# Optimization experiments

Hardware: AMD Instinct MI355X
Metric: run time of the kernel (lower is better)

The kernel has to match this reference:

```python
import jax, jax.numpy as jnp
import numpy as np

N, E = 50000, 800000
IN_DIM, HID, HEADS, OUT_DIM, EDGE_DIM = 128, 32, 4, 64, 32


def _glorot(key, shape, dtype=jnp.float32):
    fan_in, fan_out = shape[0], shape[1]
    lim = np.sqrt(6.0 / (fan_in + fan_out))
    return jax.random.uniform(key, shape, dtype, -lim, lim)


def setup_inputs() -> dict:
    key = jax.random.key(0)
    ks = jax.random.split(key, 16)
    H1 = HEADS * HID  # 128 = concat width of layer 1
    inp = {
        "x": jax.random.normal(ks[0], (N, IN_DIM), jnp.float32),
        "edge_index": jax.random.randint(ks[1], (2, E), 0, N, jnp.int64),
        "edge_feats": jax.random.normal(ks[2], (E, EDGE_DIM), jnp.float32),
        # layer 1: TransformerConv(128 -> 32, heads=4, concat=True, edge_dim=32)
        "Wq1": _glorot(ks[3], (IN_DIM, H1)), "bq1": jnp.zeros((H1,), jnp.float32),
        "Wk1": _glorot(ks[4], (IN_DIM, H1)), "bk1": jnp.zeros((H1,), jnp.float32),
        "Wv1": _glorot(ks[5], (IN_DIM, H1)), "bv1": jnp.zeros((H1,), jnp.float32),
        "We1": _glorot(ks[6], (EDGE_DIM, H1)),
        "Ws1": _glorot(ks[7], (IN_DIM, H1)), "bs1": jnp.zeros((H1,), jnp.float32),
        # layer 2: TransformerConv(128 -> 64, heads=1, concat=False, edge_dim=32)
        "Wq2": _glorot(ks[8], (H1, OUT_DIM)), "bq2": jnp.zeros((OUT_DIM,), jnp.float32),
        "Wk2": _glorot(ks[9], (H1, OUT_DIM)), "bk2": jnp.zeros((OUT_DIM,), jnp.float32),
        "Wv2": _glorot(ks[10], (H1, OUT_DIM)), "bv2": jnp.zeros((OUT_DIM,), jnp.float32),
        "We2": _glorot(ks[11], (EDGE_DIM, OUT_DIM)),
        "Ws2": _glorot(ks[12], (H1, OUT_DIM)), "bs2": jnp.zeros((OUT_DIM,), jnp.float32),
    }
    return inp


def _tconv(x, src, dst, e, Wq, bq, Wk, bk, Wv, bv, We, Ws, bs, heads, concat):
    """PyG TransformerConv: gather q_i/k_j/v_j, add edge embedding to k and v,
    segment-softmax over incoming edges of each target node, scatter-aggregate."""
    n = x.shape[0]
    d = Wq.shape[1] // heads
    q = (x @ Wq + bq).reshape(n, heads, d)
    k = (x @ Wk + bk).reshape(n, heads, d)
    v = (x @ Wv + bv).reshape(n, heads, d)
    ee = (e @ We).reshape(-1, heads, d)      # [E, H, D]
    kj = k[src] + ee                          # [E, H, D]
    vj = v[src] + ee                          # [E, H, D]
    a = jnp.einsum('ehd,ehd->eh', q[dst], kj) / jnp.sqrt(jnp.asarray(d, x.dtype))
    amax = jax.ops.segment_max(a, dst, num_segments=n)      # [N, H]
    ex = jnp.exp(a - amax[dst])
    den = jax.ops.segment_sum(ex, dst, num_segments=n)
    alpha = ex / den[dst]                                   # [E, H]
    out = jax.ops.segment_sum(alpha[..., None] * vj, dst, num_segments=n)
    out = out.reshape(n, heads * d) if concat else out.mean(axis=1)
    return out + x @ Ws + bs  # root/skip connection (lin_skip)


def reference(x, edge_index, edge_feats,
              Wq1, bq1, Wk1, bk1, Wv1, bv1, We1, Ws1, bs1,
              Wq2, bq2, Wk2, bk2, Wv2, bv2, We2, Ws2, bs2):
    src, dst = edge_index[0], edge_index[1]  # flow='source_to_target'
    h = _tconv(x, src, dst, edge_feats, Wq1, bq1, Wk1, bk1, Wv1, bv1,
               We1, Ws1, bs1, heads=HEADS, concat=True)
    h = jax.nn.relu(h)  # activation; dropout p=0.0 is identity
    h = _tconv(h, src, dst, edge_feats, Wq2, bq2, Wk2, bk2, Wv2, bv2,
               We2, Ws2, bs2, heads=1, concat=False)
    return h
```

## Files before the change

### kernel.cpp

```cpp
#include <hip/hip_runtime.h>
#include <hip/hip_bf16.h>


typedef unsigned int  u32;
typedef unsigned short u16;
typedef __attribute__((ext_vector_type(8))) __bf16 bf16x8;
typedef __attribute__((ext_vector_type(4))) float  f32x4;

#define S1L (0.17677669529663687f * 1.4426950408889634f)
#define S2L (0.125f * 1.4426950408889634f)

__device__ __forceinline__ u16 f2bf(float f) {
    u32 u = __float_as_uint(f);
    u32 r = (u + 0x7fffu + ((u >> 16) & 1u)) >> 16;
    return (u16)r;
}
__device__ __forceinline__ float bflo(u32 u) { return __uint_as_float(u << 16); }
__device__ __forceinline__ float bfhi(u32 u) { return __uint_as_float(u & 0xffff0000u); }

template<int CTRL>
__device__ __forceinline__ float dpp_add(float x) {
    int y = __builtin_amdgcn_mov_dpp(__float_as_int(x), CTRL, 0xF, 0xF, true);
    return x + __int_as_float(y);
}

__global__ void k_hist(const int* __restrict__ dst, int* __restrict__ deg, int nE) {
    int e = blockIdx.x * 256 + threadIdx.x;
    if (e < nE) atomicAdd(&deg[dst[e]], 1);
}

__global__ __launch_bounds__(1024) void k_scan_part(const int* __restrict__ deg,
                                                    int* __restrict__ rp,
                                                    int* __restrict__ csum, int nN)
{
    __shared__ int buf[1024];
    const int tid = threadIdx.x, idx = blockIdx.x * 1024 + tid;
    int v = (idx < nN) ? deg[idx] : 0;
    buf[tid] = v;
    __syncthreads();
    for (int off = 1; off < 1024; off <<= 1) {
        int t = (tid >= off) ? buf[tid - off] : 0;
        __syncthreads();
        buf[tid] += t;
        __syncthreads();
    }
    if (idx < nN) rp[idx] = buf[tid] - v;
    if (tid == 1023) csum[blockIdx.x] = buf[1023];
}

__global__ __launch_bounds__(1024) void k_scan_tot(int* __restrict__ csum, int nb,
                                                   int* __restrict__ rowptr, int nN, int nE)
{
    __shared__ int buf[1024];
    const int tid = threadIdx.x;
    int v = (tid < nb) ? csum[tid] : 0;
    buf[tid] = v;
    __syncthreads();
    for (int off = 1; off < 1024; off <<= 1) {
        int t = (tid >= off) ? buf[tid - off] : 0;
        __syncthreads();
        buf[tid] += t;
        __syncthreads();
    }
    if (tid < nb) csum[tid] = buf[tid] - v;
    if (tid == 0) rowptr[nN] = nE;
}

__global__ void k_scan_apply(int* __restrict__ rp, const int* __restrict__ csum,
                             int* __restrict__ fill, int nN)
{
    int i = blockIdx.x * 256 + threadIdx.x;
    if (i < nN) { int r = rp[i] + csum[i >> 10]; rp[i] = r; fill[i] = r; }
}

__global__ void k_scatter(const int* __restrict__ src, const int* __restrict__ dst,
                          const float4* __restrict__ ef4,
                          int* __restrict__ fill, int* __restrict__ srcs,
                          uint2* __restrict__ efc, int nE)
{
    int e = blockIdx.x * 256 + threadIdx.x;
    if (e < nE) {
        int p = atomicAdd(&fill[dst[e]], 1);
        srcs[p] = src[e];
        const float4* r = ef4 + (size_t)e * 8;
        uint2* w = efc + (size_t)p * 8;
        #pragma unroll
        for (int t = 0; t < 8; ++t) {
            float4 f = r[t];
            w[t] = make_uint2((u32)f2bf(f.x) | ((u32)f2bf(f.y) << 16),
                              (u32)f2bf(f.z) | ((u32)f2bf(f.w) << 16));
        }
    }
}

__global__ void k_f2h4(const float4* __restrict__ in4, uint2* __restrict__ out4, long n4) {
    long i = (long)blockIdx.x * 256 + threadIdx.x;
    if (i < n4) {
        float4 f = in4[i];
        out4[i] = make_uint2((u32)f2bf(f.x) | ((u32)f2bf(f.y) << 16),
                             (u32)f2bf(f.z) | ((u32)f2bf(f.w) << 16));
    }
}

__global__ void k_w2t1(const float* __restrict__ Wq, const float* __restrict__ Wk,
                       const float* __restrict__ Wv, const float* __restrict__ Ws,
                       u16* __restrict__ WT)
{
    int t = blockIdx.x * 256 + threadIdx.x;
    if (t >= 512 * 128) return;
    int j = t >> 7, k = t & 127;
    int m = j >> 7, col = j & 127;
    const float* W = (m == 0) ? Wq : (m == 1) ? Wk : (m == 2) ? Wv : Ws;
    WT[t] = f2bf(W[k * 128 + col]);
}

__global__ void k_w2t2(const float* __restrict__ Wq, const float* __restrict__ Wk,
                       const float* __restrict__ Wv, const float* __restrict__ Ws,
                       u16* __restrict__ WT)
{
    int t = blockIdx.x * 256 + threadIdx.x;
    if (t >= 256 * 128) return;
    int j = t >> 7, k = t & 127;
    int m = j >> 6, col = j & 63;
    const float* W = (m == 0) ? Wq : (m == 1) ? Wk : (m == 2) ? Wv : Ws;
    WT[t] = f2bf(W[k * 64 + col]);
}

__global__ void k_wqe1(const float* __restrict__ Wq, const float* __restrict__ bq,
                       const float* __restrict__ We,
                       u16* __restrict__ WqET, float* __restrict__ bqe)
{
    int t = blockIdx.x * 256 + threadIdx.x;
    if (t >= 128 * 128) return;
    int j = t >> 7, m = t & 127;
    int h = j >> 5, c = j & 31;
    float acc = 0.f;
    #pragma unroll
    for (int d = 0; d < 32; ++d)
        acc += Wq[m * 128 + h * 32 + d] * We[c * 128 + h * 32 + d];
    WqET[j * 128 + m] = f2bf(acc * S1L);
    if (m == 0) {
        float b = 0.f;
        #pragma unroll
        for (int d = 0; d < 32; ++d)
            b += bq[h * 32 + d] * We[c * 128 + h * 32 + d];
        bqe[j] = b * S1L;
    }
}

__global__ void k_wqe2(const float* __restrict__ Wq, const float* __restrict__ bq,
                       const float* __restrict__ We,
                       u16* __restrict__ WqET, float* __restrict__ bqe)
{
    int t = blockIdx.x * 256 + threadIdx.x;
    if (t >= 32 * 128) return;
    int c = t >> 7, m = t & 127;
    float acc = 0.f;
    #pragma unroll
    for (int d = 0; d < 64; ++d)
        acc += Wq[m * 64 + d] * We[c * 64 + d];
    WqET[c * 128 + m] = f2bf(acc * S2L);
    if (m == 0) {
        float b = 0.f;
        #pragma unroll
        for (int d = 0; d < 64; ++d) b += bq[d] * We[c * 64 + d];
        bqe[c] = b * S2L;
    }
}

__global__ __launch_bounds__(256) void k_lin1_mfma(
    const u16* __restrict__ xb, const u16* __restrict__ WT,
    const u16* __restrict__ WqET, const float* __restrict__ bqe,
    const float* __restrict__ bq, const float* __restrict__ bk,
    const float* __restrict__ bv, const float* __restrict__ bs,
    float* __restrict__ q1, float* __restrict__ qe1,
    u32* __restrict__ kv1, float* __restrict__ sk1, int nN)
{
    const int wave = threadIdx.x >> 6, lane = threadIdx.x & 63;
    const int rowbase = blockIdx.x * 64 + wave * 16;
    const int colL = lane & 15;
    const int koff = (lane >> 4) * 8;
    const int arow = rowbase + colL;
    const int arow_c = arow < nN ? arow : (nN - 1);

    bf16x8 a[4];
    #pragma unroll
    for (int kk = 0; kk < 4; ++kk)
        a[kk] = *(const bf16x8*)(xb + (size_t)arow_c * 128 + kk * 32 + koff);

    #pragma unroll
    for (int g = 0; g < 8; ++g) {
        const int co = g * 16 + colL;
        f32x4 aq = {0.f, 0.f, 0.f, 0.f}, ak = aq, av = aq, as_ = aq, ae = aq;
        #pragma unroll
        for (int kk = 0; kk < 4; ++kk) {
            const int kb = kk * 32 + koff;
            bf16x8 b0 = *(const bf16x8*)(WT + (size_t)(co)       * 128 + kb);
            bf16x8 b1 = *(const bf16x8*)(WT + (size_t)(128 + co) * 128 + kb);
            bf16x8 b2 = *(const bf16x8*)(WT + (size_t)(256 + co) * 128 + kb);
            bf16x8 b3 = *(const bf16x8*)(WT + (size_t)(384 + co) * 128 + kb);
            bf16x8 b4 = *(const bf16x8*)(WqET + (size_t)co * 128 + kb);
            aq  = __builtin_amdgcn_mfma_f32_16x16x32_bf16(a[kk], b0, aq,  0, 0, 0);
            ak  = __builtin_amdgcn_mfma_f32_16x16x32_bf16(a[kk], b1, ak,  0, 0, 0);
            av  = __builtin_amdgcn_mfma_f32_16x16x32_bf16(a[kk], b2, av,  0, 0, 0);
            as_ = __builtin_amdgcn_mfma_f32_16x16x32_bf16(a[kk], b3, as_, 0, 0, 0);
            ae  = __builtin_amdgcn_mfma_f32_16x16x32_bf16(a[kk], b4, ae,  0, 0, 0);
        }
        const float bqv = bq[co], bkv = bk[co], bvv = bv[co], bsv = bs[co];
        const float bev = bqe[co];
        #pragma unroll
        for (int i = 0; i < 4; ++i) {
            const int r = rowbase + (lane >> 4) * 4 + i;
            if (r < nN) {
                q1[(size_t)r * 128 + co]  = (aq[i] + bqv) * S1L;
                qe1[(size_t)r * 128 + co] = ae[i] + bev;
                kv1[(size_t)r * 128 + co] = (u32)f2bf(ak[i] + bkv)
                                          | ((u32)f2bf(av[i] + bvv) << 16);
                sk1[(size_t)r * 128 + co] = as_[i] + bsv;
            }
        }
    }
}

__global__ __launch_bounds__(256) void k_lin2_mfma(
    const u16* __restrict__ hb, const u16* __restrict__ WT,
    const u16* __restrict__ WqET, const float* __restrict__ bqe,
    const float* __restrict__ bq, const float* __restrict__ bk,
    const float* __restrict__ bv, const float* __restrict__ bs,
    float* __restrict__ q2, float* __restrict__ qe2,
    u32* __restrict__ kv2, float* __restrict__ sk2, int nN)
{
    const int wave = threadIdx.x >> 6, lane = threadIdx.x & 63;
    const int rowbase = blockIdx.x * 64 + wave * 16;
    const int colL = lane & 15;
    const int koff = (lane >> 4) * 8;
    const int arow = rowbase + colL;
    const int arow_c = arow < nN ? arow : (nN - 1);

    bf16x8 a[4];
    #pragma unroll
    for (int kk = 0; kk < 4; ++kk)
        a[kk] = *(const bf16x8*)(hb + (size_t)arow_c * 128 + kk * 32 + koff);

    #pragma unroll
    for (int g = 0; g < 4; ++g) {
        const int co = g * 16 + colL;
        f32x4 aq = {0.f, 0.f, 0.f, 0.f}, ak = aq, av = aq, as_ = aq;
        #pragma unroll
        for (int kk = 0; kk < 4; ++kk) {
            const int kb = kk * 32 + koff;
            bf16x8 b0 = *(const bf16x8*)(WT + (size_t)(co)       * 128 + kb);
            bf16x8 b1 = *(const bf16x8*)(WT + (size_t)(64  + co) * 128 + kb);
            bf16x8 b2 = *(const bf16x8*)(WT + (size_t)(128 + co) * 128 + kb);
            bf16x8 b3 = *(const bf16x8*)(WT + (size_t)(192 + co) * 128 + kb);
            aq  = __builtin_amdgcn_mfma_f32_16x16x32_bf16(a[kk], b0, aq,  0, 0, 0);
            ak  = __builtin_amdgcn_mfma_f32_16x16x32_bf16(a[kk], b1, ak,  0, 0, 0);
            av  = __builtin_amdgcn_mfma_f32_16x16x32_bf16(a[kk], b2, av,  0, 0, 0);
            as_ = __builtin_amdgcn_mfma_f32_16x16x32_bf16(a[kk], b3, as_, 0, 0, 0);
        }
        const float bqv = bq[co], bkv = bk[co], bvv = bv[co], bsv = bs[co];
        #pragma unroll
        for (int i = 0; i < 4; ++i) {
            const int r = rowbase + (lane >> 4) * 4 + i;
            if (r < nN) {
                q2[(size_t)r * 64 + co]  = (aq[i] + bqv) * S2L;
                kv2[(size_t)r * 64 + co] = (u32)f2bf(ak[i] + bkv)
                                         | ((u32)f2bf(av[i] + bvv) << 16);
                sk2[(size_t)r * 64 + co] = as_[i] + bsv;
            }
        }
    }
    #pragma unroll
    for (int g = 0; g < 2; ++g) {
        const int co = g * 16 + colL;
        f32x4 ae = {0.f, 0.f, 0.f, 0.f};
        #pragma unroll
        for (int kk = 0; kk < 4; ++kk) {
            const int kb = kk * 32 + koff;
            bf16x8 b4 = *(const bf16x8*)(WqET + (size_t)co * 128 + kb);
            ae = __builtin_amdgcn_mfma_f32_16x16x32_bf16(a[kk], b4, ae, 0, 0, 0);
        }
        const float bev = bqe[co];
        #pragma unroll
        for (int i = 0; i < 4; ++i) {
            const int r = rowbase + (lane >> 4) * 4 + i;
            if (r < nN) qe2[(size_t)r * 32 + co] = ae[i] + bev;
        }
    }
}

__global__ __launch_bounds__(256) void k_agg1(
    const int* __restrict__ rowptr, const int* __restrict__ srcs,
    const u16* __restrict__ efc, const float* __restrict__ q1,
    const float* __restrict__ qe1, const u32* __restrict__ kv1,
    float* __restrict__ sv1, float* __restrict__ sef1, float* __restrict__ den1, int nN)
{
    const int wave = threadIdx.x >> 6, lane = threadIdx.x & 63;
    const int d = blockIdx.x * 4 + wave;
    if (d >= nN) return;
    const int es = lane >> 5;
    const int h  = (lane >> 3) & 3;
    const int c8 = lane & 7;
    const int jb = h * 32 + c8 * 4;

    const float4 qr  = *(const float4*)(q1  + (size_t)d * 128 + jb);
    const float4 qer = *(const float4*)(qe1 + (size_t)d * 128 + jb);

    const int beg = rowptr[d], end = rowptr[d + 1];
    float den = 0.f;
    float4 sv = {0.f, 0.f, 0.f, 0.f}, sef = sv;

    #pragma unroll 2
    for (int i = beg; i < end; i += 2) {
        const int ie = i + es;
        const bool valid = ie < end;
        const int iec = valid ? ie : beg;
        const int s = srcs[iec];
        const uint4 kp = *(const uint4*)(kv1 + ((u32)s << 7) + jb);
        const uint2 ee = *(const uint2*)(efc + ((size_t)iec << 5) + c8 * 4);
        const float f0 = bflo(ee.x), f1 = bfhi(ee.x);
        const float f2 = bflo(ee.y), f3 = bfhi(ee.y);
        float p = qr.x * bflo(kp.x) + qr.y * bflo(kp.y)
                + qr.z * bflo(kp.z) + qr.w * bflo(kp.w)
                + qer.x * f0 + qer.y * f1 + qer.z * f2 + qer.w * f3;
        p = dpp_add<0xB1>(p);
        p = dpp_add<0x4E>(p);
        p = dpp_add<0x141>(p);
        const float ex = valid ? exp2f(p) : 0.f;
        den += ex;
        sv.x += ex * bfhi(kp.x); sv.y += ex * bfhi(kp.y);
        sv.z += ex * bfhi(kp.z); sv.w += ex * bfhi(kp.w);
        sef.x += ex * f0; sef.y += ex * f1; sef.z += ex * f2; sef.w += ex * f3;
    }
    den  += __shfl_xor(den, 32);
    sv.x += __shfl_xor(sv.x, 32); sv.y += __shfl_xor(sv.y, 32);
    sv.z += __shfl_xor(sv.z, 32); sv.w += __shfl_xor(sv.w, 32);
    sef.x += __shfl_xor(sef.x, 32); sef.y += __shfl_xor(sef.y, 32);
    sef.z += __shfl_xor(sef.z, 32); sef.w += __shfl_xor(sef.w, 32);
    if (es == 0) {
        *(float4*)(sv1  + (size_t)d * 128 + jb) = sv;
        *(float4*)(sef1 + (size_t)d * 128 + jb) = sef;
        if (c8 == 0) den1[(size_t)d * 4 + h] = den;
    }
}

__global__ __launch_bounds__(256) void k_finalize1(
    const float* __restrict__ sv1, const float* __restrict__ sef1,
    const float* __restrict__ den1, const float* __restrict__ sk1,
    const float* __restrict__ We, u16* __restrict__ h1b, int nN)
{
    const int tid = threadIdx.x;
    const int g = tid >> 7, j = tid & 127, h = j >> 5;
    float wreg[32];
    #pragma unroll
    for (int cc = 0; cc < 32; ++cc) wreg[cc] = We[cc * 128 + j];
    for (int n = blockIdx.x * 2 + g; n < nN; n += gridDim.x * 2) {
        float dd = den1[(size_t)n * 4 + h];
        float acc = sv1[(size_t)n * 128 + j];
        const float* sefp = &sef1[(size_t)n * 128 + h * 32];
        #pragma unroll
        for (int cc = 0; cc < 32; ++cc) acc = fmaf(sefp[cc], wreg[cc], acc);
        float o = (dd > 0.f ? acc / dd : 0.f) + sk1[(size_t)n * 128 + j];
        h1b[(size_t)n * 128 + j] = f2bf(o > 0.f ? o : 0.f);
    }
}

__global__ __launch_bounds__(256) void k_agg2(
    const int* __restrict__ rowptr, const int* __restrict__ srcs,
    const u16* __restrict__ efc, const float* __restrict__ q2,
    const float* __restrict__ qe2, const u32* __restrict__ kv2,
    float* __restrict__ sv2, float* __restrict__ sef2, float* __restrict__ den2, int nN)
{
    const int wave = threadIdx.x >> 6, lane = threadIdx.x & 63;
    const int d = blockIdx.x * 4 + wave;
    if (d >= nN) return;
    const int es  = lane >> 4;
    const int c16 = lane & 15;
    const int jb  = c16 * 4;
    const int ce  = (c16 & 7) * 4;

    const float4 qr = *(const float4*)(q2 + (size_t)d * 64 + jb);
    float4 qer = {0.f, 0.f, 0.f, 0.f};
    if (c16 < 8) qer = *(const float4*)(qe2 + (size_t)d * 32 + jb);

    const int beg = rowptr[d], end = rowptr[d + 1];
    float den = 0.f;
    float4 sv = {0.f, 0.f, 0.f, 0.f}, sef = sv;

    #pragma unroll 2
    for (int i = beg; i < end; i += 4) {
        const int ie = i + es;
        const bool valid = ie < end;
        const int iec = valid ? ie : beg;
        const int s = srcs[iec];
        const uint4 kp = *(const uint4*)(kv2 + ((u32)s << 6) + jb);
        const uint2 ee = *(const uint2*)(efc + ((size_t)iec << 5) + ce);
        const float f0 = bflo(ee.x), f1 = bfhi(ee.x);
        const float f2 = bflo(ee.y), f3 = bfhi(ee.y);
        float p = qr.x * bflo(kp.x) + qr.y * bflo(kp.y)
                + qr.z * bflo(kp.z) + qr.w * bflo(kp.w)
                + qer.x * f0 + qer.y * f1 + qer.z * f2 + qer.w * f3;
        p = dpp_add<0xB1>(p);
        p = dpp_add<0x4E>(p);
        p = dpp_add<0x141>(p);
        p = dpp_add<0x140>(p);
        const float ex = valid ? exp2f(p) : 0.f;
        den += ex;
        sv.x += ex * bfhi(kp.x); sv.y += ex * bfhi(kp.y);
        sv.z += ex * bfhi(kp.z); sv.w += ex * bfhi(kp.w);
        sef.x += ex * f0; sef.y += ex * f1; sef.z += ex * f2; sef.w += ex * f3;
    }
    #pragma unroll
    for (int m = 16; m <= 32; m <<= 1) {
        den  += __shfl_xor(den, m);
        sv.x += __shfl_xor(sv.x, m); sv.y += __shfl_xor(sv.y, m);
        sv.z += __shfl_xor(sv.z, m); sv.w += __shfl_xor(sv.w, m);
        sef.x += __shfl_xor(sef.x, m); sef.y += __shfl_xor(sef.y, m);
        sef.z += __shfl_xor(sef.z, m); sef.w += __shfl_xor(sef.w, m);
    }
    if (es == 0) {
        *(float4*)(sv2 + (size_t)d * 64 + jb) = sv;
        if (c16 < 8) *(float4*)(sef2 + (size_t)d * 32 + jb) = sef;
        if (c16 == 0) den2[d] = den;
    }
}

__global__ __launch_bounds__(256) void k_finalize2(
    const float* __restrict__ sv2, const float* __restrict__ sef2,
    const float* __restrict__ den2, const float* __restrict__ sk2,
    const float* __restrict__ We, float* __restrict__ out, int nN)
{
    const int tid = threadIdx.x;
    const int g = tid >> 6, c = tid & 63;
    float wreg[32];
    #pragma unroll
    for (int k = 0; k < 32; ++k) wreg[k] = We[k * 64 + c];
    for (int n = blockIdx.x * 4 + g; n < nN; n += gridDim.x * 4) {
        float dd = den2[n];
        float acc = sv2[(size_t)n * 64 + c];
        const float* sefp = &sef2[(size_t)n * 32];
        #pragma unroll
        for (int k = 0; k < 32; ++k) acc = fmaf(sefp[k], wreg[k], acc);
        out[(size_t)n * 64 + c] = (dd > 0.f ? acc / dd : 0.f) + sk2[(size_t)n * 64 + c];
    }
}

extern "C" void kernel_launch(void* const* d_in, const int* in_sizes, int n_in,
                              void* d_out, int out_size, void* d_ws, size_t ws_size,
                              hipStream_t stream)
{
    const float* x   = (const float*)d_in[0];
    const int*   ei  = (const int*)d_in[1];
    const float* ef  = (const float*)d_in[2];
    const float* Wq1 = (const float*)d_in[3];  const float* bq1 = (const float*)d_in[4];
    const float* Wk1 = (const float*)d_in[5];  const float* bk1 = (const float*)d_in[6];
    const float* Wv1 = (const float*)d_in[7];  const float* bv1 = (const float*)d_in[8];
    const float* We1 = (const float*)d_in[9];
    const float* Ws1 = (const float*)d_in[10]; const float* bs1 = (const float*)d_in[11];
    const float* Wq2 = (const float*)d_in[12]; const float* bq2 = (const float*)d_in[13];
    const float* Wk2 = (const float*)d_in[14]; const float* bk2 = (const float*)d_in[15];
    const float* Wv2 = (const float*)d_in[16]; const float* bv2 = (const float*)d_in[17];
    const float* We2 = (const float*)d_in[18];
    const float* Ws2 = (const float*)d_in[19]; const float* bs2 = (const float*)d_in[20];

    const int nN = in_sizes[0] / 128;
    const int nE = in_sizes[1] / 2;
    const int* srcv = ei;
    const int* dstv = ei + nE;

    float* ws = (float*)d_ws;
    size_t off = 0;
    auto alloc = [&](size_t n) { float* p = ws + off; off += n; return p; };
    float* q1    = alloc((size_t)nN * 128);
    float* sk1   = alloc((size_t)nN * 128);
    float* qe1   = alloc((size_t)nN * 128);
    u32*   kv1   = (u32*)alloc((size_t)nN * 128);
    float* sv1   = alloc((size_t)nN * 128);
    float* sef1  = alloc((size_t)nN * 128);
    u16*   h1b   = (u16*)alloc((size_t)nN * 64);
    u16*   xb    = (u16*)alloc((size_t)nN * 64);
    float* den1  = alloc((size_t)nN * 4);
    u16*   efc   = (u16*)alloc((size_t)nE * 16);
    u16*   WT1   = (u16*)alloc(512 * 128 / 2);
    u16*   WT2   = (u16*)alloc(256 * 128 / 2);
    u16*   WqET1 = (u16*)alloc(128 * 128 / 2);
    u16*   WqET2 = (u16*)alloc(32 * 128 / 2);
    float* bqe1  = alloc(128);
    float* bqe2  = alloc(32);
    int* deg     = (int*)alloc(nN);
    int* rowptr  = (int*)alloc(nN + 1);
    int* fill    = (int*)alloc(nN);
    int* csum    = (int*)alloc(1024);
    int* srcs    = (int*)alloc(nE);
    float* l2 = q1;
    size_t o2 = 0;
    auto alloc2 = [&](size_t n) { float* p = l2 + o2; o2 += n; return p; };
    float* q2   = alloc2((size_t)nN * 64);
    u32*   kv2  = (u32*)alloc2((size_t)nN * 64);
    float* sk2  = alloc2((size_t)nN * 64);
    float* qe2  = alloc2((size_t)nN * 32);
    float* sv2  = alloc2((size_t)nN * 64);
    float* sef2 = alloc2((size_t)nN * 32);
    float* den2 = alloc2(nN);
    (void)ws_size; (void)n_in; (void)out_size;

    const int nChunk = (nN + 1023) / 1024;
    const int gemmBlocks = (nN + 63) / 64;

    hipMemsetAsync(deg, 0, (size_t)nN * sizeof(int), stream);
    k_hist<<<(nE + 255) / 256, 256, 0, stream>>>(dstv, deg, nE);
    k_scan_part<<<nChunk, 1024, 0, stream>>>(deg, rowptr, csum, nN);
    k_scan_tot<<<1, 1024, 0, stream>>>(csum, nChunk, rowptr, nN, nE);
    k_scan_apply<<<(nN + 255) / 256, 256, 0, stream>>>(rowptr, csum, fill, nN);
    k_scatter<<<(nE + 255) / 256, 256, 0, stream>>>(
        srcv, dstv, (const float4*)ef, fill, srcs, (uint2*)efc, nE);

    k_w2t1<<<(512 * 128 + 255) / 256, 256, 0, stream>>>(Wq1, Wk1, Wv1, Ws1, WT1);
    k_w2t2<<<(256 * 128 + 255) / 256, 256, 0, stream>>>(Wq2, Wk2, Wv2, Ws2, WT2);
    k_wqe1<<<(128 * 128 + 255) / 256, 256, 0, stream>>>(Wq1, bq1, We1, WqET1, bqe1);
    k_wqe2<<<(32 * 128 + 255) / 256, 256, 0, stream>>>(Wq2, bq2, We2, WqET2, bqe2);
    long nx4 = (long)nN * 32;
    k_f2h4<<<(int)((nx4 + 255) / 256), 256, 0, stream>>>((const float4*)x, (uint2*)xb, nx4);

    k_lin1_mfma<<<gemmBlocks, 256, 0, stream>>>(
        xb, WT1, WqET1, bqe1, bq1, bk1, bv1, bs1, q1, qe1, kv1, sk1, nN);
    k_agg1<<<(nN + 3) / 4, 256, 0, stream>>>(
        rowptr, srcs, efc, q1, qe1, kv1, sv1, sef1, den1, nN);
    k_finalize1<<<1024, 256, 0, stream>>>(sv1, sef1, den1, sk1, We1, h1b, nN);

    k_lin2_mfma<<<gemmBlocks, 256, 0, stream>>>(
        h1b, WT2, WqET2, bqe2, bq2, bk2, bv2, bs2, q2, qe2, kv2, sk2, nN);
    k_agg2<<<(nN + 3) / 4, 256, 0, stream>>>(
        rowptr, srcs, efc, q2, qe2, kv2, sv2, sef2, den2, nN);
    k_finalize2<<<1024, 256, 0, stream>>>(sv2, sef2, den2, sk2, We2, (float*)d_out, nN);
}
```

Baseline: 430.8 us.

## Pack layer-1 q and qe into bf16 pairs, defer GEMM stores, widen scatter writes

Layer-1 q and q·We projections are now stored as one packed bf16 pair per element instead of two fp32 arrays, which halves that traffic in both the GEMM epilogue and the aggregation gather. Both MFMA projection kernels buffer their outputs in registers and write them after all tiles are computed, and they get a launch-bounds occupancy hint. The edge-feature scatter writes 16-byte vectors instead of 8-byte ones. In exchange, q loses precision by moving to bf16, and the register buffers raise register pressure.

```diff
diff --git a/kernel.cpp b/kernel.cpp
--- a/kernel.cpp
+++ b/kernel.cpp
@@ -76,19 +76,21 @@
 __global__ void k_scatter(const int* __restrict__ src, const int* __restrict__ dst,
                           const float4* __restrict__ ef4,
                           int* __restrict__ fill, int* __restrict__ srcs,
-                          uint2* __restrict__ efc, int nE)
+                          uint4* __restrict__ efc, int nE)
 {
     int e = blockIdx.x * 256 + threadIdx.x;
     if (e < nE) {
         int p = atomicAdd(&fill[dst[e]], 1);
         srcs[p] = src[e];
         const float4* r = ef4 + (size_t)e * 8;
-        uint2* w = efc + (size_t)p * 8;
-        #pragma unroll
-        for (int t = 0; t < 8; ++t) {
-            float4 f = r[t];
-            w[t] = make_uint2((u32)f2bf(f.x) | ((u32)f2bf(f.y) << 16),
-                              (u32)f2bf(f.z) | ((u32)f2bf(f.w) << 16));
+        uint4* w = efc + (size_t)p * 4;
+        #pragma unroll
+        for (int t = 0; t < 4; ++t) {
+            float4 f0 = r[2 * t], f1 = r[2 * t + 1];
+            w[t] = make_uint4((u32)f2bf(f0.x) | ((u32)f2bf(f0.y) << 16),
+                              (u32)f2bf(f0.z) | ((u32)f2bf(f0.w) << 16),
+                              (u32)f2bf(f1.x) | ((u32)f2bf(f1.y) << 16),
+                              (u32)f2bf(f1.z) | ((u32)f2bf(f1.w) << 16));
         }
     }
 }
@@ -168,13 +170,12 @@
     }
 }
 
-__global__ __launch_bounds__(256) void k_lin1_mfma(
+__global__ __launch_bounds__(256, 2) void k_lin1_mfma(
     const u16* __restrict__ xb, const u16* __restrict__ WT,
     const u16* __restrict__ WqET, const float* __restrict__ bqe,
     const float* __restrict__ bq, const float* __restrict__ bk,
     const float* __restrict__ bv, const float* __restrict__ bs,
-    float* __restrict__ q1, float* __restrict__ qe1,
-    u32* __restrict__ kv1, float* __restrict__ sk1, int nN)
+    u32* __restrict__ qqe1, u32* __restrict__ kv1, float* __restrict__ sk1, int nN)
 {
     const int wave = threadIdx.x >> 6, lane = threadIdx.x & 63;
     const int rowbase = blockIdx.x * 64 + wave * 16;
@@ -187,6 +188,8 @@
     #pragma unroll
     for (int kk = 0; kk < 4; ++kk)
         a[kk] = *(const bf16x8*)(xb + (size_t)arow_c * 128 + kk * 32 + koff);
+
+    u32 o_qqe[8][4]; u32 o_kv[8][4]; float o_sk[8][4];
 
     #pragma unroll
     for (int g = 0; g < 8; ++g) {
@@ -210,19 +213,30 @@
         const float bev = bqe[co];
         #pragma unroll
         for (int i = 0; i < 4; ++i) {
-            const int r = rowbase + (lane >> 4) * 4 + i;
-            if (r < nN) {
-                q1[(size_t)r * 128 + co]  = (aq[i] + bqv) * S1L;
-                qe1[(size_t)r * 128 + co] = ae[i] + bev;
-                kv1[(size_t)r * 128 + co] = (u32)f2bf(ak[i] + bkv)
-                                          | ((u32)f2bf(av[i] + bvv) << 16);
-                sk1[(size_t)r * 128 + co] = as_[i] + bsv;
+            o_qqe[g][i] = (u32)f2bf((aq[i] + bqv) * S1L)
+                        | ((u32)f2bf(ae[i] + bev) << 16);
+            o_kv[g][i]  = (u32)f2bf(ak[i] + bkv) | ((u32)f2bf(av[i] + bvv) << 16);
+            o_sk[g][i]  = as_[i] + bsv;
+        }
+    }
+
+    const int rb = rowbase + (lane >> 4) * 4;
+    #pragma unroll
+    for (int i = 0; i < 4; ++i) {
+        const int r = rb + i;
+        if (r < nN) {
+            #pragma unroll
+            for (int g = 0; g < 8; ++g) {
+                const int co = g * 16 + colL;
+                qqe1[(size_t)r * 128 + co] = o_qqe[g][i];
+                kv1 [(size_t)r * 128 + co] = o_kv[g][i];
+                sk1 [(size_t)r * 128 + co] = o_sk[g][i];
             }
         }
     }
 }
 
-__global__ __launch_bounds__(256) void k_lin2_mfma(
+__global__ __launch_bounds__(256, 2) void k_lin2_mfma(
     const u16* __restrict__ hb, const u16* __restrict__ WT,
     const u16* __restrict__ WqET, const float* __restrict__ bqe,
     const float* __restrict__ bq, const float* __restrict__ bk,
@@ -241,6 +255,8 @@
     #pragma unroll
     for (int kk = 0; kk < 4; ++kk)
         a[kk] = *(const bf16x8*)(hb + (size_t)arow_c * 128 + kk * 32 + koff);
+
+    float o_q[4][4]; u32 o_kv[4][4]; float o_sk[4][4]; float o_qe[2][4];
 
     #pragma unroll
     for (int g = 0; g < 4; ++g) {
@@ -261,13 +277,9 @@
         const float bqv = bq[co], bkv = bk[co], bvv = bv[co], bsv = bs[co];
         #pragma unroll
         for (int i = 0; i < 4; ++i) {
-            const int r = rowbase + (lane >> 4) * 4 + i;
-            if (r < nN) {
-                q2[(size_t)r * 64 + co]  = (aq[i] + bqv) * S2L;
-                kv2[(size_t)r * 64 + co] = (u32)f2bf(ak[i] + bkv)
-                                         | ((u32)f2bf(av[i] + bvv) << 16);
-                sk2[(size_t)r * 64 + co] = as_[i] + bsv;
-            }
+            o_q[g][i]  = (aq[i] + bqv) * S2L;
+            o_kv[g][i] = (u32)f2bf(ak[i] + bkv) | ((u32)f2bf(av[i] + bvv) << 16);
+            o_sk[g][i] = as_[i] + bsv;
         }
     }
     #pragma unroll
@@ -282,17 +294,32 @@
         }
         const float bev = bqe[co];
         #pragma unroll
-        for (int i = 0; i < 4; ++i) {
-            const int r = rowbase + (lane >> 4) * 4 + i;
-            if (r < nN) qe2[(size_t)r * 32 + co] = ae[i] + bev;
+        for (int i = 0; i < 4; ++i) o_qe[g][i] = ae[i] + bev;
+    }
+
+    const int rb = rowbase + (lane >> 4) * 4;
+    #pragma unroll
+    for (int i = 0; i < 4; ++i) {
+        const int r = rb + i;
+        if (r < nN) {
+            #pragma unroll
+            for (int g = 0; g < 4; ++g) {
+                const int co = g * 16 + colL;
+                q2 [(size_t)r * 64 + co] = o_q[g][i];
+                kv2[(size_t)r * 64 + co] = o_kv[g][i];
+                sk2[(size_t)r * 64 + co] = o_sk[g][i];
+            }
+            #pragma unroll
+            for (int g = 0; g < 2; ++g)
+                qe2[(size_t)r * 32 + g * 16 + colL] = o_qe[g][i];
         }
     }
 }
 
 __global__ __launch_bounds__(256) void k_agg1(
     const int* __restrict__ rowptr, const int* __restrict__ srcs,
-    const u16* __restrict__ efc, const float* __restrict__ q1,
-    const float* __restrict__ qe1, const u32* __restrict__ kv1,
+    const u16* __restrict__ efc, const u32* __restrict__ qqe1,
+    const u32* __restrict__ kv1,
     float* __restrict__ sv1, float* __restrict__ sef1, float* __restrict__ den1, int nN)
 {
     const int wave = threadIdx.x >> 6, lane = threadIdx.x & 63;
@@ -303,8 +330,9 @@
     const int c8 = lane & 7;
     const int jb = h * 32 + c8 * 4;
 
-    const float4 qr  = *(const float4*)(q1  + (size_t)d * 128 + jb);
-    const float4 qer = *(const float4*)(qe1 + (size_t)d * 128 + jb);
+    const uint4 qq = *(const uint4*)(qqe1 + (size_t)d * 128 + jb);
+    const float4 qr  = {bflo(qq.x), bflo(qq.y), bflo(qq.z), bflo(qq.w)};
+    const float4 qer = {bfhi(qq.x), bfhi(qq.y), bfhi(qq.z), bfhi(qq.w)};
 
     const int beg = rowptr[d], end = rowptr[d + 1];
     float den = 0.f;
@@ -471,9 +499,8 @@
     float* ws = (float*)d_ws;
     size_t off = 0;
     auto alloc = [&](size_t n) { float* p = ws + off; off += n; return p; };
-    float* q1    = alloc((size_t)nN * 128);
+    u32*   qqe1  = (u32*)alloc((size_t)nN * 128);
     float* sk1   = alloc((size_t)nN * 128);
-    float* qe1   = alloc((size_t)nN * 128);
     u32*   kv1   = (u32*)alloc((size_t)nN * 128);
     float* sv1   = alloc((size_t)nN * 128);
     float* sef1  = alloc((size_t)nN * 128);
@@ -492,7 +519,7 @@
     int* fill    = (int*)alloc(nN);
     int* csum    = (int*)alloc(1024);
     int* srcs    = (int*)alloc(nE);
-    float* l2 = q1;
+    float* l2 = (float*)qqe1;
     size_t o2 = 0;
     auto alloc2 = [&](size_t n) { float* p = l2 + o2; o2 += n; return p; };
     float* q2   = alloc2((size_t)nN * 64);
@@ -513,7 +540,7 @@
     k_scan_tot<<<1, 1024, 0, stream>>>(csum, nChunk, rowptr, nN, nE);
     k_scan_apply<<<(nN + 255) / 256, 256, 0, stream>>>(rowptr, csum, fill, nN);
     k_scatter<<<(nE + 255) / 256, 256, 0, stream>>>(
-        srcv, dstv, (const float4*)ef, fill, srcs, (uint2*)efc, nE);
+        srcv, dstv, (const float4*)ef, fill, srcs, (uint4*)efc, nE);
 
     k_w2t1<<<(512 * 128 + 255) / 256, 256, 0, stream>>>(Wq1, Wk1, Wv1, Ws1, WT1);
     k_w2t2<<<(256 * 128 + 255) / 256, 256, 0, stream>>>(Wq2, Wk2, Wv2, Ws2, WT2);
@@ -523,9 +550,9 @@
     k_f2h4<<<(int)((nx4 + 255) / 256), 256, 0, stream>>>((const float4*)x, (uint2*)xb, nx4);
 
     k_lin1_mfma<<<gemmBlocks, 256, 0, stream>>>(
-        xb, WT1, WqET1, bqe1, bq1, bk1, bv1, bs1, q1, qe1, kv1, sk1, nN);
+        xb, WT1, WqET1, bqe1, bq1, bk1, bv1, bs1, qqe1, kv1, sk1, nN);
     k_agg1<<<(nN + 3) / 4, 256, 0, stream>>>(
-        rowptr, srcs, efc, q1, qe1, kv1, sv1, sef1, den1, nN);
+        rowptr, srcs, efc, qqe1, kv1, sv1, sef1, den1, nN);
     k_finalize1<<<1024, 256, 0, stream>>>(sv1, sef1, den1, sk1, We1, h1b, nN);
 
     k_lin2_mfma<<<gemmBlocks, 256, 0, stream>>>(
```

Result: no change. 432.5 us (+0.4%).
